# Optimization experiments

Measured on AMD Instinct MI355X. Metric: run time of the kernel, lower is better.

Reference implementation:

```python
import jax, jax.numpy as jnp
import numpy as np
import math

B, C, H, W, D = 4, 64, 16, 16, 16
TEMB = 256
GROUPS = 16
EPS = 1e-5


def group_norm(x, gamma, beta, groups=GROUPS, eps=EPS):
    # x: [B, C, H, W, D]
    b, c, h, w, d = x.shape
    xg = x.reshape(b, groups, c // groups, h, w, d)
    mu = jnp.mean(xg, axis=(2, 3, 4, 5), keepdims=True)
    var = jnp.var(xg, axis=(2, 3, 4, 5), keepdims=True)
    xn = ((xg - mu) / jnp.sqrt(var + eps)).reshape(b, c, h, w, d)
    return xn * gamma[None, :, None, None, None] + beta[None, :, None, None, None]


def swish(x):
    return x * jax.nn.sigmoid(x)


def conv3d(x, w, b=None):
    y = jax.lax.conv_general_dilated(
        x, w, window_strides=(1, 1, 1), padding='SAME',
        dimension_numbers=('NCDHW', 'OIDHW', 'NCDHW'))
    if b is not None:
        y = y + b[None, :, None, None, None]
    return y


def setup_inputs() -> dict:
    key = jax.random.key(0)
    ks = jax.random.split(key, 16)
    s = lambda fan: 1.0 / math.sqrt(fan)
    inp = {
        'x': jax.random.normal(ks[0], (B, C, H, W, D), jnp.float32),
        'time_emb': jax.random.normal(ks[1], (B, TEMB), jnp.float32),
        # block1: GroupNorm + Conv3d(C->C, 3)
        'gn1_g': jnp.ones((C,), jnp.float32),
        'gn1_b': jnp.zeros((C,), jnp.float32),
        'conv1_w': jax.random.normal(ks[2], (C, C, 3, 3, 3), jnp.float32) * s(C * 27),
        'conv1_b': jnp.zeros((C,), jnp.float32),
        # time-embedding MLP: Linear(TEMB -> C)
        'mlp_w': jax.random.normal(ks[3], (C, TEMB), jnp.float32) * s(TEMB),
        'mlp_b': jnp.zeros((C,), jnp.float32),
        # block2: GroupNorm + Conv3d(C->C, 3)
        'gn2_g': jnp.ones((C,), jnp.float32),
        'gn2_b': jnp.zeros((C,), jnp.float32),
        'conv2_w': jax.random.normal(ks[4], (C, C, 3, 3, 3), jnp.float32) * s(C * 27),
        'conv2_b': jnp.zeros((C,), jnp.float32),
        # attention: GroupNorm, qkv 1x1 conv (no bias), out 1x1 conv
        'agn_g': jnp.ones((C,), jnp.float32),
        'agn_b': jnp.zeros((C,), jnp.float32),
        'qkv_w': jax.random.normal(ks[5], (3 * C, C), jnp.float32) * s(C),
        'out_w': jax.random.normal(ks[6], (C, C), jnp.float32) * s(C),
        'out_b': jnp.zeros((C,), jnp.float32),
    }
    return inp


def reference(x, time_emb, gn1_g, gn1_b, conv1_w, conv1_b, mlp_w, mlp_b,
              gn2_g, gn2_b, conv2_w, conv2_b, agn_g, agn_b, qkv_w, out_w, out_b):
    # --- ResnetBlock ---
    h = conv3d(swish(group_norm(x, gn1_g, gn1_b)), conv1_w, conv1_b)
    t = swish(time_emb) @ mlp_w.T + mlp_b                    # [B, C]
    h = h + t[:, :, None, None, None]
    h = conv3d(swish(group_norm(h, gn2_g, gn2_b)), conv2_w, conv2_b)
    x = h + x                                                # res_conv is Identity (dim == dim_out)
    # --- SelfAttention (n_head = 1) ---
    b, c, hh, ww, dd = x.shape
    n = hh * ww * dd
    norm = group_norm(x, agn_g, agn_b)
    qkv = jnp.einsum('oc,bchwd->bohwd', qkv_w, norm).reshape(b, 3 * c, n)
    q, k, v = jnp.split(qkv, 3, axis=1)                      # [B, C, N] each
    attn = jnp.einsum('bcn,bcm->bnm', q, k) / math.sqrt(c)   # [B, N, N]
    attn = jax.nn.softmax(attn, axis=-1)
    o = jnp.einsum('bnm,bcm->bcn', attn, v).reshape(b, c, hh, ww, dd)
    o = jnp.einsum('oc,bchwd->bohwd', out_w, o) + out_b[None, :, None, None, None]
    return o + x
```

## Files before the change

### kernel.cpp

```cpp
#include <hip/hip_runtime.h>
#include <math.h>

#define B 4
#define C 64
#define G 16
#define CPG 4
#define N 4096
#define TEMB 256

using f16x8 = __attribute__((ext_vector_type(8))) _Float16;
using f16x4 = __attribute__((ext_vector_type(4))) _Float16;
using f32x4 = __attribute__((ext_vector_type(4))) float;
using f32x16 = __attribute__((ext_vector_type(16))) float;
using h2 = __attribute__((ext_vector_type(2))) __fp16;

#define QSCALE 0.18033688f
#define SHIFT2 4.328085f

__device__ __forceinline__ int swzi(int row, int ci) {
  return (((ci >> 3) ^ (row & 7)) << 3) | (ci & 7);
}

__device__ __forceinline__ void gn_fin(const float2* pstats, const float* gamma,
                                       const float* beta, int b, int c,
                                       float& sc, float& sh) {
  int g = c >> 2;
  const float2* ps = pstats + ((size_t)(b * 16 + g)) * 4;
  float2 p0 = ps[0], p1 = ps[1], p2 = ps[2], p3 = ps[3];
  const float inv = 1.f / 16384.f;
  float mean = (p0.x + p1.x + p2.x + p3.x) * inv;
  float msq = (p0.y + p1.y + p2.y + p3.y) * inv;
  float var = msq - mean * mean;
  float rstd = rsqrtf(var + 1e-5f);
  sc = gamma[c] * rstd;
  sh = beta[c] - mean * sc;
}

__global__ void __launch_bounds__(256) k_gnpart(const float* __restrict__ x,
                                                float2* __restrict__ pstats) {
  int bx = blockIdx.x;
  const float4* xp = (const float4*)(x + (size_t)bx * 4096);
  float s = 0.f, s2 = 0.f;
#pragma unroll
  for (int kk = 0; kk < 4; kk++) {
    float4 v = xp[threadIdx.x + kk * 256];
    s += v.x + v.y + v.z + v.w;
    s2 += v.x * v.x + v.y * v.y + v.z * v.z + v.w * v.w;
  }
#pragma unroll
  for (int off = 32; off > 0; off >>= 1) {
    s += __shfl_down(s, off);
    s2 += __shfl_down(s2, off);
  }
  __shared__ float ls[4], ls2[4];
  int lane = threadIdx.x & 63, wid = threadIdx.x >> 6;
  if (lane == 0) { ls[wid] = s; ls2[wid] = s2; }
  __syncthreads();
  if (threadIdx.x == 0) {
    float2 r;
    r.x = ls[0] + ls[1] + ls[2] + ls[3];
    r.y = ls2[0] + ls2[1] + ls2[2] + ls2[3];
    pstats[bx] = r;
  }
}

__global__ void __launch_bounds__(256) k_prep(const float* __restrict__ w1,
                                              const float* __restrict__ w2,
                                              const float* __restrict__ temb,
                                              const float* __restrict__ mlp_w,
                                              const float* __restrict__ mlp_b,
                                              _Float16* __restrict__ wf1,
                                              _Float16* __restrict__ wf2,
                                              float* __restrict__ tb) {
  int bx = blockIdx.x, tid = threadIdx.x;
  if (bx < 54) {
    const float* w = (bx < 27) ? w1 : w2;
    _Float16* wf = (bx < 27) ? wf1 : wf2;
    int tap = (bx < 27) ? bx : bx - 27;
    int co = tid >> 2, ci0 = (tid & 3) * 16;
    union { _Float16 hh[16]; f16x8 v[2]; } pk;
#pragma unroll
    for (int r = 0; r < 16; r++)
      pk.hh[r] = (_Float16)w[((size_t)(co * 64 + ci0 + r)) * 27 + tap];
    f16x8* dst = (f16x8*)(wf + ((size_t)tap * 64 + co) * 64 + ci0);
    dst[0] = pk.v[0]; dst[1] = pk.v[1];
  } else {
    int b = bx - 54;
    __shared__ float sw[TEMB];
    __shared__ float part[4][64];
    {
      float v = temb[b * TEMB + tid];
      sw[tid] = v / (1.f + __expf(-v));
    }
    __syncthreads();
    int co = tid & 63, seg = tid >> 6;
    float acc = 0.f;
#pragma unroll 16
    for (int k = 0; k < 64; k++) acc += sw[seg * 64 + k] * mlp_w[co * TEMB + seg * 64 + k];
    part[seg][co] = acc;
    __syncthreads();
    if (tid < 64) tb[b * C + tid] = part[0][tid] + part[1][tid] + part[2][tid] + part[3][tid] + mlp_b[tid];
  }
}

__global__ void __launch_bounds__(256) k_actT(const float* __restrict__ in,
                                              const float2* __restrict__ pstats,
                                              const float* __restrict__ gamma,
                                              const float* __restrict__ beta,
                                              _Float16* __restrict__ outT) {
  int b = blockIdx.x >> 6, nt = blockIdx.x & 63;
  int n0 = nt * 64;
  __shared__ float xl[64][68];
  int tid = threadIdx.x;
  {
    int c = tid >> 2, seg = tid & 3;
    float sc, sh;
    gn_fin(pstats, gamma, beta, b, c, sc, sh);
    const float4* src = (const float4*)(in + ((size_t)(b * C + c)) * N + n0 + seg * 16);
#pragma unroll
    for (int j = 0; j < 4; j++) {
      float4 v = src[j];
      float t0 = v.x * sc + sh, t1 = v.y * sc + sh, t2 = v.z * sc + sh, t3 = v.w * sc + sh;
      xl[c][seg * 16 + j * 4 + 0] = t0 / (1.f + __expf(-t0));
      xl[c][seg * 16 + j * 4 + 1] = t1 / (1.f + __expf(-t1));
      xl[c][seg * 16 + j * 4 + 2] = t2 / (1.f + __expf(-t2));
      xl[c][seg * 16 + j * 4 + 3] = t3 / (1.f + __expf(-t3));
    }
  }
  __syncthreads();
  {
    int n = tid >> 2, cq = (tid & 3) * 16;
    union { _Float16 hh[16]; f16x8 v[2]; } pk;
#pragma unroll
    for (int r = 0; r < 16; r++) pk.hh[r] = (_Float16)xl[cq + r][n];
    f16x8* dst = (f16x8*)(outT + ((size_t)b * N + n0 + n) * 64 + cq);
    dst[0] = pk.v[0]; dst[1] = pk.v[1];
  }
}

__global__ void __launch_bounds__(256) k_conv3(const _Float16* __restrict__ actT,
                                               const _Float16* __restrict__ wf,
                                               const float* __restrict__ bias,
                                               const float* __restrict__ addvec,
                                               const float* __restrict__ residual,
                                               float* __restrict__ out) {
  int bx = blockIdx.x;
  int b = bx >> 6, h = (bx >> 2) & 15, nog = bx & 3;
  int tid = threadIdx.x;
  int wv = tid >> 6, lane = tid & 63, hi = lane >> 5, l31 = lane & 31;
  int cw = wv >> 1, nw = wv & 1;
  __shared__ _Float16 a3[3][96][64];
  __shared__ _Float16 wl[2][64][64];
  int w0 = nog * 4 - 1;
  for (int idx = tid; idx < 2304; idx += 256) {
    int r = idx / 768, rem = idx % 768;
    int ns = rem >> 3, ci8 = rem & 7;
    int wp = w0 + (ns >> 4), dp = ns & 15;
    int hin = h + r - 1;
    f16x8 v = {};
    if ((unsigned)hin < 16u && (unsigned)wp < 16u)
      v = *(const f16x8*)(actT + (((size_t)(b * 16 + hin)) * 256 + wp * 16 + dp) * 64 + ci8 * 8);
    *(f16x8*)&a3[r][ns][swzi(ns, ci8 * 8)] = v;
  }
#pragma unroll
  for (int q = 0; q < 2; q++) {
    int chunk = tid + q * 256;
    int co = chunk >> 3, ci8 = chunk & 7;
    f16x8 v = *(const f16x8*)(wf + (size_t)co * 64 + ci8 * 8);
    *(f16x8*)&wl[0][co][swzi(co, ci8 * 8)] = v;
  }
  f32x16 acc = {};
  __syncthreads();
  int cur = 0;
  int co_r = cw * 32 + l31;
  int n_loc = nw * 32 + l31;
  int wrow = n_loc >> 4;
  int d = n_loc & 15;
  for (int t = 0; t < 27; t++) {
    f16x8 pw0 = {}, pw1 = {};
    if (t < 26) {
      pw0 = *(const f16x8*)(wf + ((size_t)(t + 1) * 64 + (tid >> 3)) * 64 + (tid & 7) * 8);
      pw1 = *(const f16x8*)(wf + ((size_t)(t + 1) * 64 + ((tid + 256) >> 3)) * 64 + (tid & 7) * 8);
    }
    int kw = (t / 3) % 3, kd = t % 3, kh = t / 9;
    int wpl = wrow + kw;
    int dp = d + kd - 1;
    bool ok = (unsigned)dp < 16u;
    int ns = wpl * 16 + dp;
#pragma unroll
    for (int c4 = 0; c4 < 4; c4++) {
      int ci = c4 * 16 + hi * 8;
      f16x8 af = *(const f16x8*)&wl[cur][co_r][swzi(co_r, ci)];
      f16x8 bf = {};
      if (ok) bf = *(const f16x8*)&a3[kh][ns][swzi(ns, ci)];
      acc = __builtin_amdgcn_mfma_f32_32x32x16_f16(af, bf, acc, 0, 0, 0);
    }
    if (t < 26) {
      *(f16x8*)&wl[cur ^ 1][tid >> 3][swzi(tid >> 3, (tid & 7) * 8)] = pw0;
      *(f16x8*)&wl[cur ^ 1][(tid + 256) >> 3][swzi((tid + 256) >> 3, (tid & 7) * 8)] = pw1;
      __syncthreads();
      cur ^= 1;
    }
  }
  int nq = nog * 64 + n_loc;
#pragma unroll
  for (int r = 0; r < 16; r++) {
    int co = cw * 32 + (r & 3) + 8 * (r >> 2) + 4 * hi;
    size_t off = (((size_t)(b * 64 + co)) * 16 + h) * 256 + nq;
    float vv = acc[r] + bias[co] + (addvec ? addvec[b * 64 + co] : 0.f);
    if (residual) vv += residual[off];
    out[off] = vv;
  }
}

__global__ void __launch_bounds__(256) k_qkv(const float* __restrict__ x2,
                                             const float2* __restrict__ pstats,
                                             const float* __restrict__ gamma,
                                             const float* __restrict__ beta,
                                             const float* __restrict__ w,
                                             _Float16* __restrict__ qh, _Float16* __restrict__ kh,
                                             _Float16* __restrict__ vh) {
  int b = blockIdx.x >> 6, nt = blockIdx.x & 63;
  int n0 = nt * 64;
  __shared__ __align__(16) float xl[64][64];
  __shared__ float wl[192 * 64];
  int tid = threadIdx.x;
  for (int i = tid; i < 192 * 64; i += 256) wl[i] = w[i];
  {
    int c = tid >> 2, seg = tid & 3;
    float sc, sh;
    gn_fin(pstats, gamma, beta, b, c, sc, sh);
    const float4* src = (const float4*)(x2 + ((size_t)(b * C + c)) * N + n0);
    float4* dst = (float4*)&xl[c][seg * 16];
#pragma unroll
    for (int j = 0; j < 4; j++) {
      float4 v = src[seg * 4 + j];
      v.x = v.x * sc + sh; v.y = v.y * sc + sh; v.z = v.z * sc + sh; v.w = v.w * sc + sh;
      dst[j] = v;
    }
  }
  __syncthreads();
  int nq = tid & 15, og = tid >> 4;
  float4 acc[12];
#pragma unroll
  for (int j = 0; j < 12; j++) acc[j] = make_float4(0.f, 0.f, 0.f, 0.f);
  for (int c = 0; c < 64; c++) {
    float4 xv = *(const float4*)&xl[c][nq * 4];
#pragma unroll
    for (int j = 0; j < 12; j++) {
      float wv = wl[(og * 12 + j) * 64 + c];
      acc[j].x += wv * xv.x; acc[j].y += wv * xv.y; acc[j].z += wv * xv.z; acc[j].w += wv * xv.w;
    }
  }
#pragma unroll
  for (int j = 0; j < 12; j++) {
    int o3 = og * 12 + j;
    if (o3 >= 128) {
      f16x4 pv;
      pv[0] = (_Float16)acc[j].x; pv[1] = (_Float16)acc[j].y;
      pv[2] = (_Float16)acc[j].z; pv[3] = (_Float16)acc[j].w;
      *(f16x4*)(vh + ((size_t)(b * C + (o3 - 128))) * N + n0 + nq * 4) = pv;
    }
  }
  __syncthreads();
#pragma unroll
  for (int j = 0; j < 12; j++) {
    int o3 = og * 12 + j;
    if (o3 < 64) {
      float4 v = acc[j];
      v.x *= QSCALE; v.y *= QSCALE; v.z *= QSCALE; v.w *= QSCALE;
      *(float4*)&xl[o3][nq * 4] = v;
    }
  }
  __syncthreads();
  {
    int n_ = tid >> 2, cs = (tid & 3) * 16;
    union { _Float16 hh[16]; uint4 u[2]; } pk;
#pragma unroll
    for (int r = 0; r < 16; r++) pk.hh[r] = (_Float16)xl[cs + r][n_];
    uint4* dst = (uint4*)(qh + ((size_t)b * N + n0 + n_) * 64 + cs);
    dst[0] = pk.u[0]; dst[1] = pk.u[1];
  }
  __syncthreads();
#pragma unroll
  for (int j = 0; j < 12; j++) {
    int o3 = og * 12 + j;
    if (o3 >= 64 && o3 < 128) *(float4*)&xl[o3 - 64][nq * 4] = acc[j];
  }
  __syncthreads();
  {
    int n_ = tid >> 2, cs = (tid & 3) * 16;
    union { _Float16 hh[16]; uint4 u[2]; } pk;
#pragma unroll
    for (int r = 0; r < 16; r++) pk.hh[r] = (_Float16)xl[cs + r][n_];
    uint4* dst = (uint4*)(kh + ((size_t)b * N + n0 + n_) * 64 + cs);
    dst[0] = pk.u[0]; dst[1] = pk.u[1];
  }
}

__global__ void __launch_bounds__(256) k_attn(const _Float16* __restrict__ q,
                                              const _Float16* __restrict__ k,
                                              const _Float16* __restrict__ v,
                                              _Float16* __restrict__ po,
                                              float* __restrict__ pl) {
  int bx = blockIdx.x;
  int s = bx >> 8, b = (bx >> 6) & 3, nt = bx & 63;
  int n0 = nt * 64;
  int ks0 = s * 1024;
  int tid = threadIdx.x;
  int wv = tid >> 6, lane = tid & 63, lg = lane >> 4, ll = lane & 15;
  __shared__ float ol[64][72];
  __shared__ float lsum[4][64];
  const _Float16* qp = q + (size_t)b * N * 64;
  const _Float16* kp = k + (size_t)b * N * 64;
  const _Float16* vp = v + (size_t)b * C * N;
  f16x8 qf[4][2];
#pragma unroll
  for (int qb = 0; qb < 4; qb++)
#pragma unroll
    for (int ch = 0; ch < 2; ch++)
      qf[qb][ch] = *(const f16x8*)(qp + (size_t)(n0 + qb * 16 + ll) * 64 + ch * 32 + lg * 8);
  f32x4 oacc[4][4] = {};
  float lacc[4] = {0.f, 0.f, 0.f, 0.f};
  int key0 = ks0 + wv * 16;
  f16x8 kf0 = *(const f16x8*)(kp + (size_t)(key0 + ll) * 64 + lg * 8);
  f16x8 kf1 = *(const f16x8*)(kp + (size_t)(key0 + ll) * 64 + 32 + lg * 8);
  f16x4 vf[4];
#pragma unroll
  for (int cb = 0; cb < 4; cb++)
    vf[cb] = *(const f16x4*)(vp + (size_t)(cb * 16 + ll) * N + key0 + 4 * lg);
  for (int it = 0; it < 16; it++) {
    f32x4 sv[4];
    __builtin_amdgcn_s_setprio(1);
#pragma unroll
    for (int qb = 0; qb < 4; qb++) {
      f32x4 z = {-SHIFT2, -SHIFT2, -SHIFT2, -SHIFT2};
      z = __builtin_amdgcn_mfma_f32_16x16x32_f16(kf0, qf[qb][0], z, 0, 0, 0);
      sv[qb] = __builtin_amdgcn_mfma_f32_16x16x32_f16(kf1, qf[qb][1], z, 0, 0, 0);
    }
    __builtin_amdgcn_s_setprio(0);
    int keyn = ks0 + ((((it + 1) & 15) * 4 + wv)) * 16;
    f16x8 nk0 = *(const f16x8*)(kp + (size_t)(keyn + ll) * 64 + lg * 8);
    f16x8 nk1 = *(const f16x8*)(kp + (size_t)(keyn + ll) * 64 + 32 + lg * 8);
    f16x4 nv[4];
#pragma unroll
    for (int cb = 0; cb < 4; cb++)
      nv[cb] = *(const f16x4*)(vp + (size_t)(cb * 16 + ll) * N + keyn + 4 * lg);
    f16x4 pk[4];
#pragma unroll
    for (int qb = 0; qb < 4; qb++) {
      float e0 = exp2f(sv[qb][0]);
      float e1 = exp2f(sv[qb][1]);
      float e2 = exp2f(sv[qb][2]);
      float e3 = exp2f(sv[qb][3]);
      lacc[qb] += (e0 + e1) + (e2 + e3);
      union { h2 h[2]; f16x4 v4; } u;
      u.h[0] = __builtin_amdgcn_cvt_pkrtz(e0, e1);
      u.h[1] = __builtin_amdgcn_cvt_pkrtz(e2, e3);
      pk[qb] = u.v4;
    }
    __builtin_amdgcn_s_setprio(1);
#pragma unroll
    for (int qb = 0; qb < 4; qb++)
#pragma unroll
      for (int cb = 0; cb < 4; cb++)
        oacc[qb][cb] = __builtin_amdgcn_mfma_f32_16x16x16f16(vf[cb], pk[qb], oacc[qb][cb], 0, 0, 0);
    __builtin_amdgcn_s_setprio(0);
    kf0 = nk0; kf1 = nk1;
#pragma unroll
    for (int cb = 0; cb < 4; cb++) vf[cb] = nv[cb];
  }
#pragma unroll
  for (int qb = 0; qb < 4; qb++) {
    lacc[qb] += __shfl_xor(lacc[qb], 16);
    lacc[qb] += __shfl_xor(lacc[qb], 32);
  }
  if (lane < 16) {
#pragma unroll
    for (int qb = 0; qb < 4; qb++) lsum[wv][qb * 16 + lane] = lacc[qb];
  }
  for (int w = 0; w < 4; w++) {
    __syncthreads();
    if (wv == w) {
#pragma unroll
      for (int qb = 0; qb < 4; qb++)
#pragma unroll
        for (int cb = 0; cb < 4; cb++) {
          float* a = &ol[qb * 16 + ll][cb * 16 + 4 * lg];
          if (w == 0) {
            *(f32x4*)a = oacc[qb][cb];
          } else {
            f32x4 t = *(f32x4*)a;
            t += oacc[qb][cb];
            *(f32x4*)a = t;
          }
        }
    }
  }
  __syncthreads();
  {
    int n = tid >> 2, cq = (tid & 3) * 16;
    float lt = lsum[0][n] + lsum[1][n] + lsum[2][n] + lsum[3][n];
    float inv = 1.f / lt;
    union { _Float16 hh[16]; uint4 u[2]; } pk2;
#pragma unroll
    for (int j = 0; j < 16; j++) pk2.hh[j] = (_Float16)(ol[n][cq + j] * inv);
    uint4* dst = (uint4*)(po + ((size_t)(s * 4 + b) * N + n0 + n) * 64 + cq);
    dst[0] = pk2.u[0]; dst[1] = pk2.u[1];
    if (tid < 64)
      pl[(size_t)(s * 4 + b) * N + n0 + tid] =
          lsum[0][tid] + lsum[1][tid] + lsum[2][tid] + lsum[3][tid];
  }
}

__global__ void __launch_bounds__(256) k_outproj(const _Float16* __restrict__ po,
                                                 const float* __restrict__ pl,
                                                 const float* __restrict__ w,
                                                 const float* __restrict__ bias,
                                                 const float* __restrict__ x2,
                                                 float* __restrict__ out) {
  int b = blockIdx.x >> 6, nt = blockIdx.x & 63;
  int n0 = nt * 64;
  __shared__ __align__(16) float wl2[64][68];
  __shared__ __align__(16) float ol[64][68];
  __shared__ float wsc[4][64];
  int tid = threadIdx.x;
  if (tid < 64) {
    float l0 = pl[((size_t)(0 * 4 + b)) * N + n0 + tid];
    float l1 = pl[((size_t)(1 * 4 + b)) * N + n0 + tid];
    float l2 = pl[((size_t)(2 * 4 + b)) * N + n0 + tid];
    float l3 = pl[((size_t)(3 * 4 + b)) * N + n0 + tid];
    float inv = 1.f / (l0 + l1 + l2 + l3);
    wsc[0][tid] = l0 * inv; wsc[1][tid] = l1 * inv;
    wsc[2][tid] = l2 * inv; wsc[3][tid] = l3 * inv;
  }
  for (int i = tid; i < 4096; i += 256) wl2[i >> 6][i & 63] = w[i];
  __syncthreads();
  for (int i = tid; i < 4096; i += 256) {
    int n = i >> 6, c = i & 63;
    float acc = 0.f;
#pragma unroll
    for (int s = 0; s < 4; s++)
      acc += (float)po[((size_t)(s * 4 + b) * N + n0 + n) * 64 + c] * wsc[s][n];
    ol[n][c] = acc;
  }
  __syncthreads();
  int co = tid & 63, ng = tid >> 6;
  float acc16[16];
#pragma unroll
  for (int i = 0; i < 16; i++) acc16[i] = 0.f;
  for (int c4 = 0; c4 < 16; c4++) {
    float4 wv = *(const float4*)&wl2[co][c4 * 4];
#pragma unroll
    for (int i = 0; i < 16; i++) {
      float4 ov = *(const float4*)&ol[ng * 16 + i][c4 * 4];
      acc16[i] += wv.x * ov.x + wv.y * ov.y + wv.z * ov.z + wv.w * ov.w;
    }
  }
  float bv = bias[co];
  __syncthreads();
#pragma unroll
  for (int i = 0; i < 16; i++) ol[ng * 16 + i][co] = acc16[i] + bv;
  __syncthreads();
  for (int kk = 0; kk < 16; kk++) {
    int i = tid + kk * 256;
    int c2 = i >> 6, nl = i & 63;
    size_t idx = ((size_t)(b * C + c2)) * N + n0 + nl;
    out[idx] = ol[nl][c2] + x2[idx];
  }
}

extern "C" void kernel_launch(void* const* d_in, const int* in_sizes, int n_in,
                              void* d_out, int out_size, void* d_ws, size_t ws_size,
                              hipStream_t stream) {
  (void)in_sizes; (void)n_in; (void)out_size; (void)ws_size;
  const float* x       = (const float*)d_in[0];
  const float* temb    = (const float*)d_in[1];
  const float* gn1_g   = (const float*)d_in[2];
  const float* gn1_b   = (const float*)d_in[3];
  const float* conv1_w = (const float*)d_in[4];
  const float* conv1_b = (const float*)d_in[5];
  const float* mlp_w   = (const float*)d_in[6];
  const float* mlp_b   = (const float*)d_in[7];
  const float* gn2_g   = (const float*)d_in[8];
  const float* gn2_b   = (const float*)d_in[9];
  const float* conv2_w = (const float*)d_in[10];
  const float* conv2_b = (const float*)d_in[11];
  const float* agn_g   = (const float*)d_in[12];
  const float* agn_b   = (const float*)d_in[13];
  const float* qkv_w   = (const float*)d_in[14];
  const float* out_w   = (const float*)d_in[15];
  const float* out_b   = (const float*)d_in[16];
  float* out = (float*)d_out;
  float* ws = (float*)d_ws;
  const size_t F = 1048576;
  float* h        = ws;
  _Float16* qh    = (_Float16*)(ws + F);
  _Float16* khb   = qh + F;
  _Float16* vhb   = khb + F;
  float2* pst1 = (float2*)(vhb + F);
  float2* pst2 = pst1 + 256;
  float2* pst3 = pst2 + 256;
  float* tb    = (float*)(pst3 + 256);
  _Float16* wf1 = (_Float16*)(tb + 256);
  _Float16* wf2 = wf1 + 27 * 64 * 64;
  _Float16* actT = wf2 + 27 * 64 * 64;
  _Float16* po   = actT;
  float* pl      = (float*)(po + 4 * F);

  k_prep<<<58, 256, 0, stream>>>(conv1_w, conv2_w, temb, mlp_w, mlp_b, wf1, wf2, tb);
  k_gnpart<<<256, 256, 0, stream>>>(x, pst1);
  k_actT<<<256, 256, 0, stream>>>(x, pst1, gn1_g, gn1_b, actT);
  k_conv3<<<256, 256, 0, stream>>>(actT, wf1, conv1_b, tb, nullptr, h);
  k_gnpart<<<256, 256, 0, stream>>>(h, pst2);
  k_actT<<<256, 256, 0, stream>>>(h, pst2, gn2_g, gn2_b, actT);
  k_conv3<<<256, 256, 0, stream>>>(actT, wf2, conv2_b, nullptr, x, h);
  k_gnpart<<<256, 256, 0, stream>>>(h, pst3);
  k_qkv<<<256, 256, 0, stream>>>(h, pst3, agn_g, agn_b, qkv_w, qh, khb, vhb);
  k_attn<<<1024, 256, 0, stream>>>(qh, khb, vhb, po, pl);
  k_outproj<<<256, 256, 0, stream>>>(po, pl, out_w, out_b, h, out);
}
```

Baseline: 137.5 us.

## Tile V into 16-key blocks and compute softmax row sums via MFMA

The QKV projection now writes V in a tiled layout [b][keytile][c][16], so each attention wave reads a contiguous 512-byte block per key tile instead of 16 rows strided by N. The attention loop walks K and V with running pointer increments instead of recomputing indices. The softmax denominator is accumulated by an extra MFMA against a ones vector, which replaces the per-element VALU adds and the cross-lane shuffles. exp2f is swapped for the raw hardware exp2 builtin. The last prefetch now runs past the split, and for the final batch it may read past the K/V buffers.

```diff
diff --git a/kernel.cpp b/kernel.cpp
--- a/kernel.cpp
+++ b/kernel.cpp
@@ -259,7 +259,9 @@
       f16x4 pv;
       pv[0] = (_Float16)acc[j].x; pv[1] = (_Float16)acc[j].y;
       pv[2] = (_Float16)acc[j].z; pv[3] = (_Float16)acc[j].w;
-      *(f16x4*)(vh + ((size_t)(b * C + (o3 - 128))) * N + n0 + nq * 4) = pv;
+      int c = o3 - 128;
+      int t = (n0 >> 4) + (nq >> 2);
+      *(f16x4*)(vh + ((size_t)(b * 256 + t) * 64 + c) * 16 + (nq & 3) * 4) = pv;
     }
   }
   __syncthreads();
@@ -306,14 +308,11 @@
   int bx = blockIdx.x;
   int s = bx >> 8, b = (bx >> 6) & 3, nt = bx & 63;
   int n0 = nt * 64;
-  int ks0 = s * 1024;
   int tid = threadIdx.x;
   int wv = tid >> 6, lane = tid & 63, lg = lane >> 4, ll = lane & 15;
   __shared__ float ol[64][72];
   __shared__ float lsum[4][64];
   const _Float16* qp = q + (size_t)b * N * 64;
-  const _Float16* kp = k + (size_t)b * N * 64;
-  const _Float16* vp = v + (size_t)b * C * N;
   f16x8 qf[4][2];
 #pragma unroll
   for (int qb = 0; qb < 4; qb++)
@@ -321,15 +320,18 @@
     for (int ch = 0; ch < 2; ch++)
       qf[qb][ch] = *(const f16x8*)(qp + (size_t)(n0 + qb * 16 + ll) * 64 + ch * 32 + lg * 8);
   f32x4 oacc[4][4] = {};
-  float lacc[4] = {0.f, 0.f, 0.f, 0.f};
-  int key0 = ks0 + wv * 16;
-  f16x8 kf0 = *(const f16x8*)(kp + (size_t)(key0 + ll) * 64 + lg * 8);
-  f16x8 kf1 = *(const f16x8*)(kp + (size_t)(key0 + ll) * 64 + 32 + lg * 8);
+  f32x4 lfrag[4] = {};
+  const f16x4 ones = {(_Float16)1.f, (_Float16)1.f, (_Float16)1.f, (_Float16)1.f};
+  const _Float16* kptr = k + (size_t)b * N * 64 + (size_t)(s * 1024 + wv * 16 + ll) * 64 + lg * 8;
+  const _Float16* vptr = v + ((size_t)(b * 256 + s * 64 + wv) * 64 + ll) * 16 + lg * 4;
+  f16x8 kf0 = *(const f16x8*)(kptr);
+  f16x8 kf1 = *(const f16x8*)(kptr + 32);
   f16x4 vf[4];
 #pragma unroll
-  for (int cb = 0; cb < 4; cb++)
-    vf[cb] = *(const f16x4*)(vp + (size_t)(cb * 16 + ll) * N + key0 + 4 * lg);
+  for (int cb = 0; cb < 4; cb++) vf[cb] = *(const f16x4*)(vptr + cb * 256);
   for (int it = 0; it < 16; it++) {
+    const _Float16* kptrn = kptr + 4096;
+    const _Float16* vptrn = vptr + 4096;
     f32x4 sv[4];
     __builtin_amdgcn_s_setprio(1);
 #pragma unroll
@@ -339,21 +341,18 @@
       sv[qb] = __builtin_amdgcn_mfma_f32_16x16x32_f16(kf1, qf[qb][1], z, 0, 0, 0);
     }
     __builtin_amdgcn_s_setprio(0);
-    int keyn = ks0 + ((((it + 1) & 15) * 4 + wv)) * 16;
-    f16x8 nk0 = *(const f16x8*)(kp + (size_t)(keyn + ll) * 64 + lg * 8);
-    f16x8 nk1 = *(const f16x8*)(kp + (size_t)(keyn + ll) * 64 + 32 + lg * 8);
+    f16x8 nk0 = *(const f16x8*)(kptrn);
+    f16x8 nk1 = *(const f16x8*)(kptrn + 32);
     f16x4 nv[4];
 #pragma unroll
-    for (int cb = 0; cb < 4; cb++)
-      nv[cb] = *(const f16x4*)(vp + (size_t)(cb * 16 + ll) * N + keyn + 4 * lg);
+    for (int cb = 0; cb < 4; cb++) nv[cb] = *(const f16x4*)(vptrn + cb * 256);
     f16x4 pk[4];
 #pragma unroll
     for (int qb = 0; qb < 4; qb++) {
-      float e0 = exp2f(sv[qb][0]);
-      float e1 = exp2f(sv[qb][1]);
-      float e2 = exp2f(sv[qb][2]);
-      float e3 = exp2f(sv[qb][3]);
-      lacc[qb] += (e0 + e1) + (e2 + e3);
+      float e0 = __builtin_amdgcn_exp2f(sv[qb][0]);
+      float e1 = __builtin_amdgcn_exp2f(sv[qb][1]);
+      float e2 = __builtin_amdgcn_exp2f(sv[qb][2]);
+      float e3 = __builtin_amdgcn_exp2f(sv[qb][3]);
       union { h2 h[2]; f16x4 v4; } u;
       u.h[0] = __builtin_amdgcn_cvt_pkrtz(e0, e1);
       u.h[1] = __builtin_amdgcn_cvt_pkrtz(e2, e3);
@@ -361,23 +360,21 @@
     }
     __builtin_amdgcn_s_setprio(1);
 #pragma unroll
-    for (int qb = 0; qb < 4; qb++)
+    for (int qb = 0; qb < 4; qb++) {
 #pragma unroll
       for (int cb = 0; cb < 4; cb++)
         oacc[qb][cb] = __builtin_amdgcn_mfma_f32_16x16x16f16(vf[cb], pk[qb], oacc[qb][cb], 0, 0, 0);
+      lfrag[qb] = __builtin_amdgcn_mfma_f32_16x16x16f16(ones, pk[qb], lfrag[qb], 0, 0, 0);
+    }
     __builtin_amdgcn_s_setprio(0);
     kf0 = nk0; kf1 = nk1;
 #pragma unroll
     for (int cb = 0; cb < 4; cb++) vf[cb] = nv[cb];
-  }
-#pragma unroll
-  for (int qb = 0; qb < 4; qb++) {
-    lacc[qb] += __shfl_xor(lacc[qb], 16);
-    lacc[qb] += __shfl_xor(lacc[qb], 32);
+    kptr = kptrn; vptr = vptrn;
   }
   if (lane < 16) {
 #pragma unroll
-    for (int qb = 0; qb < 4; qb++) lsum[wv][qb * 16 + lane] = lacc[qb];
+    for (int qb = 0; qb < 4; qb++) lsum[wv][qb * 16 + lane] = lfrag[qb][0];
   }
   for (int w = 0; w < 4; w++) {
     __syncthreads();
```

Result: faster. 116.3 us (-15.4%).
